# Optimization experiments

Hardware: AMD Instinct MI355X
Metric: run time of the kernel (lower is better)

Reference implementation:

```python
import jax, jax.numpy as jnp
import numpy as np

B, SQ, SK, D = 8, 4096, 4096, 64


def setup_inputs() -> dict:
    key = jax.random.key(0)
    k1, k2, k3 = jax.random.split(key, 3)
    x1 = jax.random.normal(k1, (B, SQ, D), dtype=jnp.float32)   # queries
    x2 = jax.random.normal(k2, (B, SK, D), dtype=jnp.float32)   # keys
    x3 = jax.random.normal(k3, (B, SK, D), dtype=jnp.float32)   # values
    x4 = 0                                                      # dropout p (static, 0 => deterministic)
    x5 = jnp.ones((1,), dtype=jnp.float32)                      # scale divisor
    return {"x1": x1, "x2": x2, "x3": x3, "x4": x4, "x5": x5}


def reference(x1, x2, x3, x4, x5):
    # scores: [B, Sq, Sk]
    scores = jnp.einsum("bqd,bkd->bqk", x1, x2) / x5
    attn = jax.nn.softmax(scores, axis=-1)
    p = float(x4)  # static python scalar
    if p > 0.0:
        mask = jax.random.bernoulli(jax.random.key(42), 1.0 - p, attn.shape)
        attn = attn * mask.astype(attn.dtype) / (1.0 - p)
    # out: [B, Sq, D]
    return jnp.einsum("bqk,bkd->bqd", attn, x3)
```

## Files before the change

### kernel.cpp

```cpp
#include <hip/hip_runtime.h>


typedef _Float16 f16x8 __attribute__((ext_vector_type(8)));
typedef _Float16 f16x4 __attribute__((ext_vector_type(4)));
typedef __fp16   h16x2 __attribute__((ext_vector_type(2)));
typedef float    f32x4 __attribute__((ext_vector_type(4)));
typedef float    f32x16 __attribute__((ext_vector_type(16)));

constexpr int kB  = 8;
constexpr int kSQ = 4096;
constexpr int kSK = 4096;
constexpr int kD  = 64;
constexpr int KSPLIT = 4;
constexpr int SKH = kSK / KSPLIT;
constexpr int BQ  = 128;
constexpr int MT  = 2;
constexpr int BK  = 64;
constexpr int PSTR = 72;
constexpr float kLog2e = 1.44269504088896340736f;
constexpr float kDeferThr = 11.5f;

static __device__ __forceinline__ f16x4 pack4(float a, float b, float c, float d) {
    h16x2 p0 = __builtin_amdgcn_cvt_pkrtz(a, b);
    h16x2 p1 = __builtin_amdgcn_cvt_pkrtz(c, d);
    f16x4 r;
    r[0] = (_Float16)p0[0]; r[1] = (_Float16)p0[1];
    r[2] = (_Float16)p1[0]; r[3] = (_Float16)p1[1];
    return r;
}
static __device__ __forceinline__ f16x8 pack8(const float4& a, const float4& c) {
    f16x4 lo = pack4(a.x, a.y, a.z, a.w);
    f16x4 hi = pack4(c.x, c.y, c.z, c.w);
    f16x8 f;
    f[0] = lo[0]; f[1] = lo[1]; f[2] = lo[2]; f[3] = lo[3];
    f[4] = hi[0]; f[5] = hi[1]; f[6] = hi[2]; f[7] = hi[3];
    return f;
}
static __device__ __forceinline__ unsigned pkrtz_u(float a, float b) {
    union { h16x2 h; unsigned u; } cv;
    cv.h = __builtin_amdgcn_cvt_pkrtz(a, b);
    return cv.u;
}
static __device__ __forceinline__ float xhalf_max(float x) {
    union { float f; unsigned u; } uv; uv.f = x;
    auto pr = __builtin_amdgcn_permlane32_swap(uv.u, uv.u, false, false);
    union { unsigned u; float f; } r0, r1;
    r0.u = pr[0]; r1.u = pr[1];
    return fmaxf(r0.f, r1.f);
}
static __device__ __forceinline__ float max3f(float a, float b, float c) {
    return fmaxf(fmaxf(a, b), c);
}

typedef const __attribute__((address_space(1))) unsigned int* gu32p;
typedef __attribute__((address_space(3))) unsigned int* lu32p;
static __device__ __forceinline__ void gload_lds16(const void* g, void* l) {
    __builtin_amdgcn_global_load_lds((gu32p)g, (lu32p)l, 16, 0, 0);
}

#define PA_SLICE(dst, sv, rb) do {                                          \
    unsigned c0 = pkrtz_u((sv)[(rb)+0], (sv)[(rb)+1]);                      \
    unsigned c1 = pkrtz_u((sv)[(rb)+2], (sv)[(rb)+3]);                      \
    unsigned c2 = pkrtz_u((sv)[(rb)+4], (sv)[(rb)+5]);                      \
    unsigned c3 = pkrtz_u((sv)[(rb)+6], (sv)[(rb)+7]);                      \
    auto r02 = __builtin_amdgcn_permlane32_swap(c0, c2, false, false);      \
    auto r13 = __builtin_amdgcn_permlane32_swap(c1, c3, false, false);      \
    union { unsigned u[4]; f16x8 v; } _r;                                   \
    _r.u[0] = r02[0]; _r.u[1] = r13[0]; _r.u[2] = r02[1]; _r.u[3] = r13[1]; \
    dst = _r.v;                                                             \
} while (0)

__global__ __launch_bounds__(256, 2)
void fattn_prepass(const float* __restrict__ Kg,
                   const float* __restrict__ Vg,
                   _Float16* __restrict__ Kh,
                   _Float16* __restrict__ Vt)
{
    __shared__ _Float16 tr[kD][BK];

    const int tid = threadIdx.x;
    const int kt  = blockIdx.x;
    const int b   = blockIdx.y;

    const int k = tid >> 2;
    const int p = tid & 3;
    const int gk = kt * BK + k;

    {
        const float* src = Kg + ((size_t)b * kSK + gk) * kD + p * 16;
        const float4 a0 = *(const float4*)(src + 0);
        const float4 a1 = *(const float4*)(src + 4);
        const float4 a2 = *(const float4*)(src + 8);
        const float4 a3 = *(const float4*)(src + 12);
        _Float16* dst = Kh + ((size_t)b * kSK + gk) * kD;
        const int fb0 = 2 * p, fb1 = 2 * p + 1;
        *(f16x8*)&dst[(fb0 ^ (gk & 7)) * 8] = pack8(a0, a1);
        *(f16x8*)&dst[(fb1 ^ (gk & 7)) * 8] = pack8(a2, a3);
    }
    {
        const float* src = Vg + ((size_t)b * kSK + gk) * kD + p * 16;
        const float4 a0 = *(const float4*)(src + 0);
        const float4 a1 = *(const float4*)(src + 4);
        const float4 a2 = *(const float4*)(src + 8);
        const float4 a3 = *(const float4*)(src + 12);
        const float v[16] = {a0.x,a0.y,a0.z,a0.w, a1.x,a1.y,a1.z,a1.w,
                             a2.x,a2.y,a2.z,a2.w, a3.x,a3.y,a3.z,a3.w};
#pragma unroll
        for (int j = 0; j < 16; ++j)
            tr[p * 16 + j][k] = (_Float16)v[j];
    }
    __syncthreads();
    {
        const int f  = tid >> 2;
        const int p2 = tid & 3;
        const f16x8 b0 = *(const f16x8*)&tr[f][p2 * 16 + 0];
        const f16x8 b1 = *(const f16x8*)&tr[f][p2 * 16 + 8];
        _Float16* dst = Vt + (((size_t)b * 64 + kt) * kD + f) * BK;
        const int kb0 = 2 * p2, kb1 = 2 * p2 + 1;
        *(f16x8*)&dst[(kb0 ^ (f & 7)) * 8] = b0;
        *(f16x8*)&dst[(kb1 ^ (f & 7)) * 8] = b1;
    }
}

__global__ __launch_bounds__(512, 2)
void fattn_fused(const float* __restrict__ Qg,
                 const _Float16* __restrict__ Kh,
                 const _Float16* __restrict__ Vt,
                 const float* __restrict__ sdiv,
                 float* __restrict__ Og)
{
    __shared__ __align__(16) char smem[131072];
    _Float16* sKb = (_Float16*)smem;
    _Float16* sVb = (_Float16*)(smem + 65536);
    _Float16* sPart = (_Float16*)smem;
    float2*   sMl   = (float2*)(smem + (size_t)2 * 4 * 64 * PSTR * 2);

    const int tid  = threadIdx.x;
    const int w    = tid >> 6;
    const int lane = tid & 63;
    const int l31  = lane & 31;
    const int hi   = lane >> 5;
    const int ks   = w & 3;
    const int mh   = w >> 2;

    const int flat = blockIdx.x;
    const int b    = flat & 7;
    const int qi   = flat >> 3;
    const int qb   = qi * BQ;

    const float qscale = kLog2e / sdiv[0];

    const float* Qb = Qg + ((size_t)b * kSQ + qb) * kD;
    const _Float16* Khb = Kh + ((size_t)b * kSK + (size_t)ks * SKH) * kD;
    const _Float16* Vtb = Vt + (((size_t)b * 64 + (size_t)ks * (SKH / BK)) * kD) * BK;

    _Float16* sK = sKb + (ks * 2) * 4096;
    _Float16* sV = sVb + (ks * 2) * 4096;

    f16x8 qf[MT][4];
#pragma unroll
    for (int mt = 0; mt < MT; ++mt) {
        const float* qrow = Qb + (size_t)(mh * 64 + mt * 32 + l31) * kD;
#pragma unroll
        for (int ds = 0; ds < 4; ++ds) {
            const float4 a  = *(const float4*)(qrow + ds * 16 + hi * 8);
            const float4 cc = *(const float4*)(qrow + ds * 16 + hi * 8 + 4);
            float4 as = make_float4(a.x * qscale, a.y * qscale, a.z * qscale, a.w * qscale);
            float4 cs = make_float4(cc.x * qscale, cc.y * qscale, cc.z * qscale, cc.w * qscale);
            qf[mt][ds] = pack8(as, cs);
        }
    }

    f16x8 ones;
#pragma unroll
    for (int j = 0; j < 8; ++j) ones[j] = (_Float16)1.0f;
    f32x16 zacc;
#pragma unroll
    for (int r = 0; r < 16; ++r) zacc[r] = 0.0f;

    int offA[4];
#pragma unroll
    for (int i = 0; i < 4; ++i)
        offA[i] = l31 * 64 + (((2 * i + hi) ^ (l31 & 7)) * 8);

    auto stage = [&](int kt, int buf) {
        const char* gk = (const char*)(Khb + (size_t)kt * BK * kD) + mh * 4096 + lane * 16;
        const char* gv = (const char*)(Vtb + (size_t)kt * kD * BK) + mh * 4096 + lane * 16;
        char* lk = (char*)&sK[buf * 4096] + mh * 4096;
        char* lv = (char*)&sV[buf * 4096] + mh * 4096;
        gload_lds16(gk,        lk);
        gload_lds16(gk + 1024, lk + 1024);
        gload_lds16(gk + 2048, lk + 2048);
        gload_lds16(gk + 3072, lk + 3072);
        gload_lds16(gv,        lv);
        gload_lds16(gv + 1024, lv + 1024);
        gload_lds16(gv + 2048, lv + 2048);
        gload_lds16(gv + 3072, lv + 3072);
    };

    f32x16 oL[MT], oH[MT];
    f32x16 ol[MT];
    float m_i[MT];
#pragma unroll
    for (int mt = 0; mt < MT; ++mt) {
        m_i[mt] = -1e30f;
#pragma unroll
        for (int r = 0; r < 16; ++r) { oL[mt][r] = 0.0f; oH[mt][r] = 0.0f; ol[mt][r] = 0.0f; }
    }

    stage(0, 0);
    __syncthreads();

    const int nIter = SKH / BK;
    for (int kt = 0; kt < nIter; ++kt) {
        const int buf = kt & 1;
        if (kt + 1 < nIter) stage(kt + 1, buf ^ 1);

        f16x8 kf0[4], kf1[4];
#pragma unroll
        for (int ds = 0; ds < 4; ++ds) {
            kf0[ds] = *(const f16x8*)&sK[buf * 4096 + offA[ds]];
            kf1[ds] = *(const f16x8*)&sK[buf * 4096 + offA[ds] + 2048];
        }

        f32x16 s0[MT], s1[MT];
        __builtin_amdgcn_s_setprio(1);
#pragma unroll
        for (int mt = 0; mt < MT; ++mt) {
            s0[mt] = __builtin_amdgcn_mfma_f32_32x32x16_f16(kf0[0], qf[mt][0], zacc, 0, 0, 0);
            s1[mt] = __builtin_amdgcn_mfma_f32_32x32x16_f16(kf1[0], qf[mt][0], zacc, 0, 0, 0);
        }
#pragma unroll
        for (int ds = 1; ds < 4; ++ds)
#pragma unroll
            for (int mt = 0; mt < MT; ++mt) {
                s0[mt] = __builtin_amdgcn_mfma_f32_32x32x16_f16(kf0[ds], qf[mt][ds], s0[mt], 0, 0, 0);
                s1[mt] = __builtin_amdgcn_mfma_f32_32x32x16_f16(kf1[ds], qf[mt][ds], s1[mt], 0, 0, 0);
            }
        __builtin_amdgcn_s_setprio(0);

        f16x8 vf[4][2];
#pragma unroll
        for (int s = 0; s < 4; ++s) {
            vf[s][0] = *(const f16x8*)&sV[buf * 4096 + offA[s]];
            vf[s][1] = *(const f16x8*)&sV[buf * 4096 + offA[s] + 2048];
        }

#pragma unroll
        for (int mt = 0; mt < MT; ++mt) {
            float t[16];
#pragma unroll
            for (int r = 0; r < 16; ++r) t[r] = fmaxf(s0[mt][r], s1[mt][r]);
            const float u0 = max3f(t[0],  t[1],  t[2]);
            const float u1 = max3f(t[3],  t[4],  t[5]);
            const float u2 = max3f(t[6],  t[7],  t[8]);
            const float u3 = max3f(t[9],  t[10], t[11]);
            const float u4 = max3f(t[12], t[13], t[14]);
            float rm = fmaxf(max3f(u0, u1, u2), max3f(u3, u4, t[15]));
            rm = xhalf_max(rm);

            if (!__all(rm <= m_i[mt] + kDeferThr)) {
                const float mnew  = fmaxf(m_i[mt], rm);
                const float alpha = __builtin_amdgcn_exp2f(m_i[mt] - mnew);
                ol[mt][0] *= alpha;
#pragma unroll
                for (int r = 0; r < 16; ++r) { oL[mt][r] *= alpha; oH[mt][r] *= alpha; }
                m_i[mt] = mnew;
            }

#pragma unroll
            for (int r = 0; r < 16; ++r) {
                s0[mt][r] = __builtin_amdgcn_exp2f(s0[mt][r] - m_i[mt]);
                s1[mt][r] = __builtin_amdgcn_exp2f(s1[mt][r] - m_i[mt]);
            }

            f16x8 pa[4];
            PA_SLICE(pa[0], s0[mt], 0);
            PA_SLICE(pa[1], s0[mt], 8);
            PA_SLICE(pa[2], s1[mt], 0);
            PA_SLICE(pa[3], s1[mt], 8);

            __builtin_amdgcn_s_setprio(1);
#pragma unroll
            for (int s = 0; s < 4; ++s) {
                oL[mt] = __builtin_amdgcn_mfma_f32_32x32x16_f16(vf[s][0], pa[s], oL[mt], 0, 0, 0);
                oH[mt] = __builtin_amdgcn_mfma_f32_32x32x16_f16(vf[s][1], pa[s], oH[mt], 0, 0, 0);
                ol[mt] = __builtin_amdgcn_mfma_f32_32x32x16_f16(ones,     pa[s], ol[mt], 0, 0, 0);
            }
            __builtin_amdgcn_s_setprio(0);
        }

        __syncthreads();
    }

#pragma unroll
    for (int mt = 0; mt < MT; ++mt) {
        const int ql = mt * 32 + l31;
        const float lf = ol[mt][0];
        const float inv = 1.0f / lf;
        _Float16* prow = sPart + ((size_t)(mh * 4 + ks) * 64 + ql) * PSTR;
#pragma unroll
        for (int g = 0; g < 4; ++g) {
            *(f16x4*)&prow[g * 8 + hi * 4] =
                pack4(oL[mt][4 * g] * inv, oL[mt][4 * g + 1] * inv,
                      oL[mt][4 * g + 2] * inv, oL[mt][4 * g + 3] * inv);
            *(f16x4*)&prow[32 + g * 8 + hi * 4] =
                pack4(oH[mt][4 * g] * inv, oH[mt][4 * g + 1] * inv,
                      oH[mt][4 * g + 2] * inv, oH[mt][4 * g + 3] * inv);
        }
        if (hi == 0) sMl[(mh * 4 + ks) * 64 + ql] = make_float2(m_i[mt], lf);
    }
    __syncthreads();

    {
        const int qrow = tid >> 2;
        const int cc   = (tid & 3) * 16;
        const int emh  = qrow >> 6;
        const int eql  = qrow & 63;

        float2 ml[KSPLIT];
        float m = -1e30f;
#pragma unroll
        for (int s = 0; s < KSPLIT; ++s) {
            ml[s] = sMl[(emh * 4 + s) * 64 + eql];
            m = fmaxf(m, ml[s].x);
        }
        float wgt[KSPLIT];
        float lsum = 0.f;
#pragma unroll
        for (int s = 0; s < KSPLIT; ++s) {
            wgt[s] = __builtin_amdgcn_exp2f(ml[s].x - m) * ml[s].y;
            lsum += wgt[s];
        }
        const float inv = 1.0f / lsum;

        float* orow = Og + (((size_t)b * kSQ + qb + qrow)) * kD + cc;
#pragma unroll
        for (int j = 0; j < 4; ++j) {
            float a0 = 0.f, a1 = 0.f, a2 = 0.f, a3 = 0.f;
#pragma unroll
            for (int s = 0; s < KSPLIT; ++s) {
                const f16x4 a = *(const f16x4*)&sPart[((size_t)(emh * 4 + s) * 64 + eql) * PSTR + cc + j * 4];
                a0 += wgt[s] * (float)a[0];
                a1 += wgt[s] * (float)a[1];
                a2 += wgt[s] * (float)a[2];
                a3 += wgt[s] * (float)a[3];
            }
            *(float4*)&orow[j * 4] = make_float4(a0 * inv, a1 * inv, a2 * inv, a3 * inv);
        }
    }
}

extern "C" void kernel_launch(void* const* d_in, const int* in_sizes, int n_in,
                              void* d_out, int out_size, void* d_ws, size_t ws_size,
                              hipStream_t stream) {
    const float* Q    = (const float*)d_in[0];
    const float* K    = (const float*)d_in[1];
    const float* V    = (const float*)d_in[2];
    const float* sdiv = (const float*)d_in[4];
    float* O = (float*)d_out;

    _Float16* Kh  = (_Float16*)d_ws;
    _Float16* Vt  = Kh + (size_t)kB * kSK * kD;

    fattn_prepass<<<dim3(kSK / BK, kB), dim3(256), 0, stream>>>(K, V, Kh, Vt);
    fattn_fused<<<dim3(kB * (kSQ / BQ)), dim3(512), 0, stream>>>(Q, Kh, Vt, sdiv, O);
}
```

Baseline: 131.0 us.

## Load K/V fragments directly from global into registers, dropping LDS staging

Replaces the double-buffered global-to-LDS staging of K and V tiles with direct global loads of the MFMA fragments into registers, prefetching the next tile's K after the QK MFMAs and its V after the PV MFMAs. This removes the per-iteration __syncthreads and the LDS round trip, and shrinks shared memory to just the split-K combine buffers. Launch bounds drop to one block per SM, which allows more registers for the prefetched fragments. The cost is that the two wave-halves (mh) now each fetch the same K/V data from global/L2 with no sharing through LDS, and global load latency must be hidden by a single iteration of compute at lower occupancy.

After: 168.6 us. +28.7%, slower.

```diff
diff --git a/kernel.cpp b/kernel.cpp
--- a/kernel.cpp
+++ b/kernel.cpp
@@ -52,12 +52,6 @@
     return fmaxf(fmaxf(a, b), c);
 }
 
-typedef const __attribute__((address_space(1))) unsigned int* gu32p;
-typedef __attribute__((address_space(3))) unsigned int* lu32p;
-static __device__ __forceinline__ void gload_lds16(const void* g, void* l) {
-    __builtin_amdgcn_global_load_lds((gu32p)g, (lu32p)l, 16, 0, 0);
-}
-
 #define PA_SLICE(dst, sv, rb) do {                                          \
     unsigned c0 = pkrtz_u((sv)[(rb)+0], (sv)[(rb)+1]);                      \
     unsigned c1 = pkrtz_u((sv)[(rb)+2], (sv)[(rb)+3]);                      \
@@ -122,18 +116,15 @@
     }
 }
 
-__global__ __launch_bounds__(512, 2)
+__global__ __launch_bounds__(512, 1)
 void fattn_fused(const float* __restrict__ Qg,
                  const _Float16* __restrict__ Kh,
                  const _Float16* __restrict__ Vt,
                  const float* __restrict__ sdiv,
                  float* __restrict__ Og)
 {
-    __shared__ __align__(16) char smem[131072];
-    _Float16* sKb = (_Float16*)smem;
-    _Float16* sVb = (_Float16*)(smem + 65536);
-    _Float16* sPart = (_Float16*)smem;
-    float2*   sMl   = (float2*)(smem + (size_t)2 * 4 * 64 * PSTR * 2);
+    __shared__ __align__(16) _Float16 sPart[8][64][PSTR];
+    __shared__ float2 sMl[8][64];
 
     const int tid  = threadIdx.x;
     const int w    = tid >> 6;
@@ -154,9 +145,6 @@
     const _Float16* Khb = Kh + ((size_t)b * kSK + (size_t)ks * SKH) * kD;
     const _Float16* Vtb = Vt + (((size_t)b * 64 + (size_t)ks * (SKH / BK)) * kD) * BK;
 
-    _Float16* sK = sKb + (ks * 2) * 4096;
-    _Float16* sV = sVb + (ks * 2) * 4096;
-
     f16x8 qf[MT][4];
 #pragma unroll
     for (int mt = 0; mt < MT; ++mt) {
@@ -174,29 +162,11 @@
     f16x8 ones;
 #pragma unroll
     for (int j = 0; j < 8; ++j) ones[j] = (_Float16)1.0f;
-    f32x16 zacc;
-#pragma unroll
-    for (int r = 0; r < 16; ++r) zacc[r] = 0.0f;
 
     int offA[4];
 #pragma unroll
     for (int i = 0; i < 4; ++i)
         offA[i] = l31 * 64 + (((2 * i + hi) ^ (l31 & 7)) * 8);
-
-    auto stage = [&](int kt, int buf) {
-        const char* gk = (const char*)(Khb + (size_t)kt * BK * kD) + mh * 4096 + lane * 16;
-        const char* gv = (const char*)(Vtb + (size_t)kt * kD * BK) + mh * 4096 + lane * 16;
-        char* lk = (char*)&sK[buf * 4096] + mh * 4096;
-        char* lv = (char*)&sV[buf * 4096] + mh * 4096;
-        gload_lds16(gk,        lk);
-        gload_lds16(gk + 1024, lk + 1024);
-        gload_lds16(gk + 2048, lk + 2048);
-        gload_lds16(gk + 3072, lk + 3072);
-        gload_lds16(gv,        lv);
-        gload_lds16(gv + 1024, lv + 1024);
-        gload_lds16(gv + 2048, lv + 2048);
-        gload_lds16(gv + 3072, lv + 3072);
-    };
 
     f32x16 oL[MT], oH[MT];
     f32x16 ol[MT];
@@ -208,30 +178,33 @@
         for (int r = 0; r < 16; ++r) { oL[mt][r] = 0.0f; oH[mt][r] = 0.0f; ol[mt][r] = 0.0f; }
     }
 
-    stage(0, 0);
-    __syncthreads();
+    f16x8 kf0[4], kf1[4], vf0[4], vf1[4];
+#pragma unroll
+    for (int ds = 0; ds < 4; ++ds) {
+        kf0[ds] = *(const f16x8*)&Khb[offA[ds]];
+        kf1[ds] = *(const f16x8*)&Khb[offA[ds] + 2048];
+    }
+#pragma unroll
+    for (int s = 0; s < 4; ++s) {
+        vf0[s] = *(const f16x8*)&Vtb[offA[s]];
+        vf1[s] = *(const f16x8*)&Vtb[offA[s] + 2048];
+    }
 
     const int nIter = SKH / BK;
     for (int kt = 0; kt < nIter; ++kt) {
-        const int buf = kt & 1;
-        if (kt + 1 < nIter) stage(kt + 1, buf ^ 1);
-
-        f16x8 kf0[4], kf1[4];
-#pragma unroll
-        for (int ds = 0; ds < 4; ++ds) {
-            kf0[ds] = *(const f16x8*)&sK[buf * 4096 + offA[ds]];
-            kf1[ds] = *(const f16x8*)&sK[buf * 4096 + offA[ds] + 2048];
-        }
+        const bool more = (kt + 1 < nIter);
+        const _Float16* KhN = Khb + (size_t)(kt + 1) * (BK * kD);
+        const _Float16* VtN = Vtb + (size_t)(kt + 1) * (kD * BK);
 
         f32x16 s0[MT], s1[MT];
+#pragma unroll
+        for (int mt = 0; mt < MT; ++mt)
+#pragma unroll
+            for (int r = 0; r < 16; ++r) { s0[mt][r] = 0.0f; s1[mt][r] = 0.0f; }
+
         __builtin_amdgcn_s_setprio(1);
 #pragma unroll
-        for (int mt = 0; mt < MT; ++mt) {
-            s0[mt] = __builtin_amdgcn_mfma_f32_32x32x16_f16(kf0[0], qf[mt][0], zacc, 0, 0, 0);
-            s1[mt] = __builtin_amdgcn_mfma_f32_32x32x16_f16(kf1[0], qf[mt][0], zacc, 0, 0, 0);
-        }
-#pragma unroll
-        for (int ds = 1; ds < 4; ++ds)
+        for (int ds = 0; ds < 4; ++ds)
 #pragma unroll
             for (int mt = 0; mt < MT; ++mt) {
                 s0[mt] = __builtin_amdgcn_mfma_f32_32x32x16_f16(kf0[ds], qf[mt][ds], s0[mt], 0, 0, 0);
@@ -239,11 +212,12 @@
             }
         __builtin_amdgcn_s_setprio(0);
 
-        f16x8 vf[4][2];
-#pragma unroll
-        for (int s = 0; s < 4; ++s) {
-            vf[s][0] = *(const f16x8*)&sV[buf * 4096 + offA[s]];
-            vf[s][1] = *(const f16x8*)&sV[buf * 4096 + offA[s] + 2048];
+        if (more) {
+#pragma unroll
+            for (int ds = 0; ds < 4; ++ds) {
+                kf0[ds] = *(const f16x8*)&KhN[offA[ds]];
+                kf1[ds] = *(const f16x8*)&KhN[offA[ds] + 2048];
+            }
         }
 
 #pragma unroll
@@ -283,14 +257,20 @@
             __builtin_amdgcn_s_setprio(1);
 #pragma unroll
             for (int s = 0; s < 4; ++s) {
-                oL[mt] = __builtin_amdgcn_mfma_f32_32x32x16_f16(vf[s][0], pa[s], oL[mt], 0, 0, 0);
-                oH[mt] = __builtin_amdgcn_mfma_f32_32x32x16_f16(vf[s][1], pa[s], oH[mt], 0, 0, 0);
-                ol[mt] = __builtin_amdgcn_mfma_f32_32x32x16_f16(ones,     pa[s], ol[mt], 0, 0, 0);
+                oL[mt] = __builtin_amdgcn_mfma_f32_32x32x16_f16(vf0[s], pa[s], oL[mt], 0, 0, 0);
+                oH[mt] = __builtin_amdgcn_mfma_f32_32x32x16_f16(vf1[s], pa[s], oH[mt], 0, 0, 0);
+                ol[mt] = __builtin_amdgcn_mfma_f32_32x32x16_f16(ones,   pa[s], ol[mt], 0, 0, 0);
             }
             __builtin_amdgcn_s_setprio(0);
         }
 
-        __syncthreads();
+        if (more) {
+#pragma unroll
+            for (int s = 0; s < 4; ++s) {
+                vf0[s] = *(const f16x8*)&VtN[offA[s]];
+                vf1[s] = *(const f16x8*)&VtN[offA[s] + 2048];
+            }
+        }
     }
 
 #pragma unroll
@@ -298,7 +278,7 @@
         const int ql = mt * 32 + l31;
         const float lf = ol[mt][0];
         const float inv = 1.0f / lf;
-        _Float16* prow = sPart + ((size_t)(mh * 4 + ks) * 64 + ql) * PSTR;
+        _Float16* prow = &sPart[mh * 4 + ks][ql][0];
 #pragma unroll
         for (int g = 0; g < 4; ++g) {
             *(f16x4*)&prow[g * 8 + hi * 4] =
@@ -308,7 +288,7 @@
                 pack4(oH[mt][4 * g] * inv, oH[mt][4 * g + 1] * inv,
                       oH[mt][4 * g + 2] * inv, oH[mt][4 * g + 3] * inv);
         }
-        if (hi == 0) sMl[(mh * 4 + ks) * 64 + ql] = make_float2(m_i[mt], lf);
+        if (hi == 0) sMl[mh * 4 + ks][ql] = make_float2(m_i[mt], lf);
     }
     __syncthreads();
 
@@ -322,7 +302,7 @@
         float m = -1e30f;
 #pragma unroll
         for (int s = 0; s < KSPLIT; ++s) {
-            ml[s] = sMl[(emh * 4 + s) * 64 + eql];
+            ml[s] = sMl[emh * 4 + s][eql];
             m = fmaxf(m, ml[s].x);
         }
         float wgt[KSPLIT];
@@ -340,7 +320,7 @@
             float a0 = 0.f, a1 = 0.f, a2 = 0.f, a3 = 0.f;
 #pragma unroll
             for (int s = 0; s < KSPLIT; ++s) {
-                const f16x4 a = *(const f16x4*)&sPart[((size_t)(emh * 4 + s) * 64 + eql) * PSTR + cc + j * 4];
+                const f16x4 a = *(const f16x4*)&sPart[emh * 4 + s][eql][cc + j * 4];
                 a0 += wgt[s] * (float)a[0];
                 a1 += wgt[s] * (float)a[1];
                 a2 += wgt[s] * (float)a[2];
```
